# Performance work log

Measured on AMD Instinct MI355X. Metric: run time of the kernel, lower is better.

Reference implementation:

```python
import jax, jax.numpy as jnp
import numpy as np

IMG = 128
HW = IMG // 2          # render resolution (img_size // 2)
NPTS = 64              # samples per ray
MIN_D, MAX_D = 1.2, 2.8
VOL_PHYS = 1.0         # physical volume size; voxel = VOL_PHYS / D
B, C, D = 8, 16, 64
EPS_EA = 1e-10         # pytorch3d EmissionAbsorption eps
BN_EPS = 1e-5


def setup_inputs():
    key = jax.random.key(0)
    ks = jax.random.split(key, 6)
    R = jnp.tile(jnp.eye(3, dtype=jnp.float32)[None], (B, 1, 1))
    T = jnp.tile(jnp.array([0.0, 0.0, 2.0], jnp.float32)[None], (B, 1))
    K = jnp.tile(jnp.array([[180.0, 0.0, 64.0], [0.0, 180.0, 64.0], [0.0, 0.0, 1.0]],
                           jnp.float32)[None], (B, 1, 1))
    feature_3d = jax.random.normal(ks[0], (B, C, D, D, D), jnp.float32)
    density_3d = jax.random.uniform(ks[1], (B, 1, D, D, D), jnp.float32)
    wt = jax.random.normal(ks[2], (16, 16, 6, 6), jnp.float32) * 0.05
    bt = jnp.zeros((16,), jnp.float32)
    g1 = jnp.ones((16,), jnp.float32); be1 = jnp.zeros((16,), jnp.float32)
    w1 = jax.random.normal(ks[3], (8, 16, 5, 5), jnp.float32) * 0.05
    b1 = jnp.zeros((8,), jnp.float32)
    g2 = jnp.ones((8,), jnp.float32); be2 = jnp.zeros((8,), jnp.float32)
    w2 = jax.random.normal(ks[4], (3, 8, 5, 5), jnp.float32) * 0.05
    b2 = jnp.zeros((3,), jnp.float32)
    return dict(R=R, T=T, K=K, feature_3d=feature_3d, density_3d=density_3d,
                wt=wt, bt=bt, g1=g1, be1=be1, w1=w1, b1=b1, g2=g2, be2=be2,
                w2=w2, b2=b2)


def _trilerp(vol, pts):
    # vol [C,Dz,Dy,Dx]; pts [N,3] xyz in [-1,1]; grid_sample align_corners=True, zero padding
    Cc, Dz, Dy, Dx = vol.shape
    ix = (pts[:, 0] + 1.0) * 0.5 * (Dx - 1)
    iy = (pts[:, 1] + 1.0) * 0.5 * (Dy - 1)
    iz = (pts[:, 2] + 1.0) * 0.5 * (Dz - 1)
    x0f = jnp.floor(ix); y0f = jnp.floor(iy); z0f = jnp.floor(iz)
    fx, fy, fz = ix - x0f, iy - y0f, iz - z0f
    x0 = x0f.astype(jnp.int32); y0 = y0f.astype(jnp.int32); z0 = z0f.astype(jnp.int32)
    out = jnp.zeros((Cc, pts.shape[0]), vol.dtype)
    for dz in (0, 1):
        for dy in (0, 1):
            for dx in (0, 1):
                xc, yc, zc = x0 + dx, y0 + dy, z0 + dz
                w = ((fx if dx else 1.0 - fx) * (fy if dy else 1.0 - fy)
                     * (fz if dz else 1.0 - fz))
                valid = ((xc >= 0) & (xc < Dx) & (yc >= 0) & (yc < Dy)
                         & (zc >= 0) & (zc < Dz))
                v = vol[:, jnp.clip(zc, 0, Dz - 1), jnp.clip(yc, 0, Dy - 1),
                        jnp.clip(xc, 0, Dx - 1)]
                out = out + (w * valid) * v
    return out  # [C,N]


def _bn(x, g, b):
    m = x.mean((0, 2, 3), keepdims=True)
    v = x.var((0, 2, 3), keepdims=True)
    return g[None, :, None, None] * (x - m) * jax.lax.rsqrt(v + BN_EPS) + b[None, :, None, None]


def _leaky(x):
    return jnp.where(x >= 0, x, 0.01 * x)


def _conv(x, w, b, pad):
    y = jax.lax.conv_general_dilated(x, w, (1, 1), [(pad, pad), (pad, pad)],
                                     dimension_numbers=('NCHW', 'OIHW', 'NCHW'))
    return y + b[None, :, None, None]


def _conv_t(x, w, b):
    # torch ConvTranspose2d(k=6, stride=2, pad=2) == dilated conv with flipped, io-swapped kernel
    wf = jnp.flip(w, (-2, -1)).transpose(1, 0, 2, 3)
    y = jax.lax.conv_general_dilated(x, wf, (1, 1), [(3, 3), (3, 3)],
                                     lhs_dilation=(2, 2),
                                     dimension_numbers=('NCHW', 'OIHW', 'NCHW'))
    return y + b[None, :, None, None]


def _forward(R, T, K, feature_3d, density_3d, wt, bt, g1, be1, w1, b1, g2, be2, w2, b2):
    Bb, Cc, Dv, Hv, Wv = feature_3d.shape
    # K /= 2; K[:,-1,-1] = 1 (non-mutating)
    Kh = (K / 2.0).at[:, 2, 2].set(1.0)
    fx, fy = Kh[:, 0, 0], Kh[:, 1, 1]
    cx, cy = Kh[:, 0, 2], Kh[:, 1, 2]
    # pixel-center grid at half resolution (NDCGridRaysampler pixel centers)
    u = jnp.arange(HW, dtype=jnp.float32) + 0.5
    v = jnp.arange(HW, dtype=jnp.float32) + 0.5
    ddx = (u[None, None, :] - cx[:, None, None]) / fx[:, None, None]  # [B,1,W]
    ddy = (v[None, :, None] - cy[:, None, None]) / fy[:, None, None]  # [B,H,1]
    one = jnp.ones((1, 1, 1), jnp.float32)
    dirs_cam = jnp.stack(jnp.broadcast_arrays(ddx, ddy, one), axis=-1)  # [B,H,W,3]
    dirs_w = jnp.einsum('bji,bhwj->bhwi', R, dirs_cam)                  # R^T d
    origin = -jnp.einsum('bji,bj->bi', R, T)                            # cam center
    depths = jnp.linspace(MIN_D, MAX_D, NPTS, dtype=jnp.float32)
    pts = (origin[:, None, None, None, :]
           + dirs_w[:, :, :, None, :] * depths[None, None, None, :, None])  # [B,H,W,P,3]
    # world -> Volumes local coords (align_corners=True span: voxel*(dim-1))
    voxel = VOL_PHYS / Dv
    scale = jnp.array([2.0 / (voxel * (Wv - 1)), 2.0 / (voxel * (Hv - 1)),
                       2.0 / (voxel * (Dv - 1))], jnp.float32)
    loc = (pts * scale).reshape(Bb, -1, 3)
    vol = jnp.concatenate([feature_3d, density_3d], axis=1)  # [B,C+1,D,H,W]
    samp = jax.vmap(_trilerp)(vol, loc)                      # [B,C+1,N]
    samp = samp.reshape(Bb, Cc + 1, HW, HW, NPTS)
    feats = jnp.moveaxis(samp[:, :Cc], 1, -1)                # [B,H,W,P,C]
    sigma = samp[:, Cc]                                      # [B,H,W,P]
    # EmissionAbsorption raymarcher (shifted cumprod, shift=1)
    cp = jnp.cumprod((1.0 + EPS_EA) - sigma, axis=-1)
    absorb = jnp.concatenate([jnp.ones_like(cp[..., :1]), cp[..., :-1]], axis=-1)
    wgt = sigma * absorb
    img = jnp.einsum('bhwp,bhwpc->bhwc', wgt, feats)
    opac = 1.0 - jnp.prod(1.0 - sigma, axis=-1)
    imgs = jnp.moveaxis(img, -1, 1)        # [B,C,HW,HW]
    sil = opac[:, None]                    # [B,1,HW,HW]
    # conv refine head
    x = _conv_t(imgs, wt, bt)              # [B,16,128,128]
    x = _leaky(_bn(x, g1, be1))
    x = _conv(x, w1, b1, pad=2)
    x = _leaky(_bn(x, g2, be2))
    x = _conv(x, w2, b2, pad=2)
    imgs_out = jax.nn.relu(x)
    sil_up = jax.image.resize(sil, (Bb, 1, IMG, IMG), 'bilinear')
    return imgs_out, sil_up


def reference(R, T, K, feature_3d, density_3d, wt, bt, g1, be1, w1, b1, g2, be2, w2, b2):
    return _forward(R, T, K, feature_3d, density_3d, wt, bt, g1, be1, w1, b1,
                    g2, be2, w2, b2)
```

## Files before the change

kernel.cpp:

```cpp
#include <hip/hip_runtime.h>
#include <hip/hip_bf16.h>

typedef __hip_bfloat16 bf16;
typedef unsigned int uint;
typedef unsigned short ushort;

using frag  = __attribute__((ext_vector_type(8))) short;
using f32x4 = __attribute__((ext_vector_type(4))) float;

__device__ bf16  g_volT[8ULL*262144*16];
__device__ bf16  g_imgT[8*4096*16];
__device__ bf16  g_t1 [8*16384*16];
__device__ bf16  g_a2r[8*16384*8];
__device__ float g_sil[8*4096];
__device__ float g_part [512*32];
__device__ float g_part2[256*16];
__device__ float g_stats[96];
__device__ bf16  g_wAt[4*5*64*8];
__device__ bf16  g_wA1[13*64*8];
__device__ bf16  g_wA2[7*64*8];

__device__ __forceinline__ float bup(ushort u){ union{uint u; float f;} x; x.u = ((uint)u)<<16; return x.f; }
__device__ __forceinline__ ushort bdn(float f){ union{ bf16 h; ushort s;} v; v.h = __float2bfloat16(f); return v.s; }
__device__ __forceinline__ uint aff2(uint u, float a0, float b0, float a1, float b1){
  float x0 = bup((ushort)(u & 0xffff)), x1 = bup((ushort)(u >> 16));
  float y0 = fmaf(a0, x0, b0); y0 = y0 >= 0.f ? y0 : 0.01f*y0;
  float y1 = fmaf(a1, x1, b1); y1 = y1 >= 0.f ? y1 : 0.01f*y1;
  return (uint)bdn(y0) | ((uint)bdn(y1) << 16);
}
__device__ __forceinline__ f32x4 mf(frag a, frag b, f32x4 c){
  return __builtin_amdgcn_mfma_f32_16x16x32_bf16(a, b, c, 0, 0, 0);
}
__device__ __forceinline__ void acc2(uint u, float w, float& a, float& b){
  union { uint u; float f; } lo, hi;
  lo.u = u << 16; hi.u = u & 0xffff0000u;
  a = fmaf(w, lo.f, a); b = fmaf(w, hi.f, b);
}

__global__ __launch_bounds__(256) void k_wprep(const float* __restrict__ wt,
                                               const float* __restrict__ w1,
                                               const float* __restrict__ w2)
{
  int tid = threadIdx.x;
  for (int idx = tid; idx < 4*5*64*8; idx += 256){
    int cls = idx / 2560; int rem = idx % 2560;
    int step = rem / 512; int rem2 = rem % 512;
    int lane = rem2 >> 3, j = rem2 & 7;
    int o = lane & 15;
    int k = step*32 + (lane>>4)*8 + j;
    int tau = k >> 4, ic = k & 15;
    int dr = cls >> 1, dc = cls & 1;
    float val = 0.f;
    if (tau < 9){
      int s = tau/3, t = tau%3;
      val = wt[(ic*16 + o)*36 + (4-2*s+dr)*6 + (4-2*t+dc)];
    }
    g_wAt[idx] = __float2bfloat16(val);
  }
  for (int idx = tid; idx < 13*64*8; idx += 256){
    int step = idx / 512; int rem2 = idx % 512;
    int lane = rem2 >> 3, j = rem2 & 7;
    int o = lane & 15;
    int k = step*32 + (lane>>4)*8 + j;
    int tau = k >> 4, ic = k & 15;
    float val = (tau < 25 && o < 8) ? w1[o*400 + ic*25 + tau] : 0.f;
    g_wA1[idx] = __float2bfloat16(val);
  }
  for (int idx = tid; idx < 7*64*8; idx += 256){
    int step = idx / 512; int rem2 = idx % 512;
    int lane = rem2 >> 3, j = rem2 & 7;
    int o = lane & 15;
    int k = step*32 + (lane>>4)*8 + j;
    int tau = k >> 3, ic = k & 7;
    float val = (tau < 25 && o < 3) ? w2[o*200 + ic*25 + tau] : 0.f;
    g_wA2[idx] = __float2bfloat16(val);
  }
}

__global__ __launch_bounds__(256) void k_transpose(const float* __restrict__ feat)
{
  __shared__ float lt[4*64*17];
  int blk = blockIdx.x;
  int yq = blk & 15, z = (blk>>4)&63, b = blk>>10;
  int y0 = yq*4;
  int tid = threadIdx.x;
  int xq = tid & 15;
  #pragma unroll
  for (int it=0; it<4; ++it){
    int cy = it*16 + (tid>>4);
    int c = cy >> 2, y = cy & 3;
    const float4 vv = *(const float4*)(feat + (size_t)b*4194304 + (size_t)c*262144
                                       + z*4096 + (y0+y)*64 + xq*4);
    float* dst = &lt[(y*64 + xq*4)*17 + c];
    dst[0]=vv.x; dst[17]=vv.y; dst[34]=vv.z; dst[51]=vv.w;
  }
  __syncthreads();
  int y = tid >> 6, x = tid & 63;
  const float* row = &lt[(y*64+x)*17];
  uint pk[8];
  #pragma unroll
  for (int c2=0;c2<8;c2++)
    pk[c2] = (uint)bdn(row[2*c2]) | ((uint)bdn(row[2*c2+1])<<16);
  uint* dst = (uint*)(g_volT + ((size_t)b*262144 + z*4096 + (y0+y)*64 + x)*16);
  uint4 lo; lo.x=pk[0]; lo.y=pk[1]; lo.z=pk[2]; lo.w=pk[3];
  uint4 hi; hi.x=pk[4]; hi.y=pk[5]; hi.z=pk[6]; hi.w=pk[7];
  *(uint4*)dst = lo;
  *(uint4*)(dst+4) = hi;
}

__global__ __launch_bounds__(64) void k_render(
    const float* __restrict__ R, const float* __restrict__ T, const float* __restrict__ Kin,
    const float* __restrict__ dens)
{
  int blk  = blockIdx.x;
  int lane = threadIdx.x;
  int b  = blk & 7;
  int t  = blk >> 3;
  int py0 = (t >> 3) * 8, px0 = (t & 7) * 8;
  int h = py0 + (lane >> 3), w = px0 + (lane & 7);

  float fx = Kin[b*9+0]*0.5f, fy = Kin[b*9+4]*0.5f;
  float cx = Kin[b*9+2]*0.5f, cy = Kin[b*9+5]*0.5f;
  float u = (float)w + 0.5f, v = (float)h + 0.5f;
  float dcx = (u - cx)/fx, dcy = (v - cy)/fy;
  float Rm[9];
  #pragma unroll
  for (int i=0;i<9;i++) Rm[i] = R[b*9+i];
  float T0 = T[b*3+0], T1 = T[b*3+1], T2 = T[b*3+2];
  float dwx = Rm[0]*dcx + Rm[3]*dcy + Rm[6];
  float dwy = Rm[1]*dcx + Rm[4]*dcy + Rm[7];
  float dwz = Rm[2]*dcx + Rm[5]*dcy + Rm[8];
  float ox = -(Rm[0]*T0 + Rm[3]*T1 + Rm[6]*T2);
  float oy = -(Rm[1]*T0 + Rm[4]*T1 + Rm[7]*T2);
  float oz = -(Rm[2]*T0 + Rm[5]*T1 + Rm[8]*T2);

  const float SC = 2.0f*64.0f/63.0f;
  const float* dp = dens + (size_t)b*262144;
  const bf16* vb = g_volT + (size_t)b*262144*16;

  float vch[16];
  #pragma unroll
  for (int c=0;c<16;c++) vch[c] = 0.f;
  float Trun = 1.0f, Pop = 1.0f;

  for (int d=0; d<64; ++d){
    float depth = 1.2f + (1.6f/63.0f) * (float)d;
    float ix = (ox + dwx*depth)*SC;  ix = (ix + 1.0f)*0.5f*63.0f;
    float iy = (oy + dwy*depth)*SC;  iy = (iy + 1.0f)*0.5f*63.0f;
    float iz = (oz + dwz*depth)*SC;  iz = (iz + 1.0f)*0.5f*63.0f;
    float xf = floorf(ix), yf = floorf(iy), zf = floorf(iz);
    int x0 = (int)xf, y0 = (int)yf, z0 = (int)zf;
    float sigma = 0.f;

    bool anyv = (x0>=-1)&(x0<64)&(y0>=-1)&(y0<64)&(z0>=-1)&(z0<64);
    if (anyv){
      float fxr = ix-xf, fyr = iy-yf, fzr = iz-zf;
      int offs[8]; float cw[8];
      #pragma unroll
      for (int k=0;k<8;k++){
        int dx = k&1, dy=(k>>1)&1, dz=(k>>2)&1;
        int xc=x0+dx, yc=y0+dy, zc=z0+dz;
        bool valid = (xc>=0)&(xc<64)&(yc>=0)&(yc<64)&(zc>=0)&(zc<64);
        float wk = (dx?fxr:1.f-fxr)*(dy?fyr:1.f-fyr)*(dz?fzr:1.f-fzr);
        cw[k] = valid ? wk : 0.0f;
        int xcc = min(max(xc,0),63), ycc=min(max(yc,0),63), zcc=min(max(zc,0),63);
        offs[k] = (zcc*64 + ycc)*64 + xcc;
      }
      #pragma unroll
      for (int k=0;k<8;k++) sigma += cw[k]*dp[offs[k]];

      float wgt = sigma * Trun;
      if (wgt > 1e-7f){
        #pragma unroll
        for (int k=0;k<8;k++){
          const uint4* p = (const uint4*)(vb + (size_t)offs[k]*16);
          uint4 q0 = p[0];
          uint4 q1 = p[1];
          float wk = cw[k]*wgt;
          acc2(q0.x, wk, vch[0],  vch[1]);
          acc2(q0.y, wk, vch[2],  vch[3]);
          acc2(q0.z, wk, vch[4],  vch[5]);
          acc2(q0.w, wk, vch[6],  vch[7]);
          acc2(q1.x, wk, vch[8],  vch[9]);
          acc2(q1.y, wk, vch[10], vch[11]);
          acc2(q1.z, wk, vch[12], vch[13]);
          acc2(q1.w, wk, vch[14], vch[15]);
        }
      }
    }
    Trun *= (1.0f + 1e-10f - sigma);
    Pop  *= (1.0f - sigma);
    if (__ballot(Trun > 1e-7f) == 0ULL) break;
  }

  g_sil[b*4096 + h*64 + w] = 1.0f - Pop;
  uint pk[8];
  #pragma unroll
  for (int c2=0;c2<8;c2++)
    pk[c2] = (uint)bdn(vch[2*c2]) | ((uint)bdn(vch[2*c2+1])<<16);
  uint* dst = (uint*)(g_imgT + ((size_t)(b*4096) + h*64 + w)*16);
  uint4 lo; lo.x=pk[0]; lo.y=pk[1]; lo.z=pk[2]; lo.w=pk[3];
  uint4 hi; hi.x=pk[4]; hi.y=pk[5]; hi.z=pk[6]; hi.w=pk[7];
  *(uint4*)dst = lo;
  *(uint4*)(dst+4) = hi;
}

__global__ __launch_bounds__(256) void k_convt(const float* __restrict__ bt)
{
  __shared__ __align__(16) short tile[3*66*16];
  __shared__ float ssum[4][16], ssq[4][16];

  int blk = blockIdx.x;
  int r = blk & 63, b = blk >> 6;
  int tid = threadIdx.x;

  for (int idx = tid; idx < 396; idx += 256){
    int row3 = idx / 132; int rem = idx - row3*132;
    int c2 = rem >> 1, half = rem & 1;
    int gr = r - 1 + row3, gc = c2 - 1;
    uint4 val = make_uint4(0,0,0,0);
    if (gr>=0 && gr<64 && gc>=0 && gc<64)
      val = *(const uint4*)(g_imgT + ((size_t)(b*4096) + gr*64 + gc)*16 + half*8);
    *(uint4*)(tile + (row3*66 + c2)*16 + half*8) = val;
  }
  __syncthreads();

  int wv = tid >> 6, lane = tid & 63;
  int dr = wv >> 1, dc = wv & 1;
  int quad = lane >> 4, col = lane & 15;
  int ic0 = (quad & 1) * 8;

  f32x4 acc[4];
  #pragma unroll
  for (int n=0;n<4;n++) acc[n] = (f32x4){0.f,0.f,0.f,0.f};

  #pragma unroll
  for (int s5=0; s5<5; ++s5){
    frag a = *(const frag*)(g_wAt + ((wv*5 + s5)*64 + lane)*8);
    int tau = 2*s5 + (quad >> 1);
    if (tau > 8) tau = 0;
    int ss = tau/3, tt = tau%3;
    #pragma unroll
    for (int n=0;n<4;n++){
      int c2 = n*16 + col + tt;
      frag bf = *(const frag*)(tile + (ss*66 + c2)*16 + ic0);
      acc[n] = mf(a, bf, acc[n]);
    }
  }

  float4 bo = *(const float4*)(bt + quad*4);
  float bor[4] = {bo.x, bo.y, bo.z, bo.w};
  float sv[4] = {0,0,0,0}, qv[4] = {0,0,0,0};
  int orow = 2*r + dr;
  #pragma unroll
  for (int n=0;n<4;n++){
    int ocol = 2*(n*16 + col) + dc;
    bf16* dst = g_t1 + ((size_t)(b*128 + orow)*128 + ocol)*16 + quad*4;
    #pragma unroll
    for (int reg=0;reg<4;reg++){
      float vvv = acc[n][reg] + bor[reg];
      dst[reg] = __float2bfloat16(vvv);
      sv[reg] += vvv; qv[reg] += vvv*vvv;
    }
  }
  #pragma unroll
  for (int m=1; m<16; m<<=1){
    #pragma unroll
    for (int reg=0;reg<4;reg++){
      sv[reg] += __shfl_xor(sv[reg], m, 64);
      qv[reg] += __shfl_xor(qv[reg], m, 64);
    }
  }
  if ((lane & 15) == 0){
    #pragma unroll
    for (int reg=0;reg<4;reg++){
      ssum[wv][quad*4+reg] = sv[reg];
      ssq [wv][quad*4+reg] = qv[reg];
    }
  }
  __syncthreads();
  if (tid < 16){
    g_part[blk*32 + tid]      = ssum[0][tid]+ssum[1][tid]+ssum[2][tid]+ssum[3][tid];
    g_part[blk*32 + 16 + tid] = ssq[0][tid]+ssq[1][tid]+ssq[2][tid]+ssq[3][tid];
  }
}

__global__ __launch_bounds__(256) void k_fin1(const float* __restrict__ g,
                                              const float* __restrict__ be)
{
  __shared__ float rs[256], rq[256];
  int tid = threadIdx.x; int c = tid>>4, seg = tid&15;
  float s=0.f, q=0.f;
  for (int k=0;k<32;k++){
    int blk = seg*32+k;
    s += g_part[blk*32 + c];
    q += g_part[blk*32 + 16 + c];
  }
  rs[tid]=s; rq[tid]=q; __syncthreads();
  for (int sft=8; sft>0; sft>>=1){
    if (seg<sft){ rs[tid]+=rs[tid+sft]; rq[tid]+=rq[tid+sft]; }
    __syncthreads();
  }
  if (seg==0){
    float m = rs[tid]*(1.0f/131072.f);
    float v = rq[tid]*(1.0f/131072.f) - m*m;
    float a = g[c]*rsqrtf(v+1e-5f);
    g_stats[32+c] = a; g_stats[48+c] = be[c]-m*a;
  }
}

__global__ __launch_bounds__(256) void k_fin2(const float* __restrict__ g,
                                              const float* __restrict__ be)
{
  __shared__ float rs[256], rq[256];
  int tid = threadIdx.x; int seg = tid & 31, c = tid >> 5;
  float s=0.f, q=0.f;
  for (int k=0;k<8;k++){
    int blk = seg*8+k;
    s += g_part2[blk*16 + c];
    q += g_part2[blk*16 + 8 + c];
  }
  rs[tid]=s; rq[tid]=q; __syncthreads();
  for (int sft=16; sft>0; sft>>=1){
    if (seg<sft){ rs[tid]+=rs[tid+sft]; rq[tid]+=rq[tid+sft]; }
    __syncthreads();
  }
  if (seg==0){
    float m = rs[tid]*(1.0f/131072.f);
    float v = rq[tid]*(1.0f/131072.f) - m*m;
    float a = g[c]*rsqrtf(v+1e-5f);
    g_stats[80+c] = a; g_stats[88+c] = be[c]-m*a;
  }
}

__global__ __launch_bounds__(256) void k_conv1(const float* __restrict__ b1)
{
  __shared__ __align__(16) short tile[8*132*16];
  __shared__ float ssum[4][8], ssq[4][8];

  int blk = blockIdx.x;
  int rt = blk & 31, b = blk >> 5;
  int tid = threadIdx.x;

  float pa[16], pb[16];
  #pragma unroll
  for (int c=0;c<16;c++){ pa[c] = g_stats[32+c]; pb[c] = g_stats[48+c]; }

  for (int it=0; it<5; ++it){
    int idx = it*256 + tid;
    if (idx < 1056){
      int r8 = idx / 132; int c2 = idx - r8*132;
      int gr = rt*4 - 2 + r8, gc = c2 - 2;
      uint4 v0 = make_uint4(0,0,0,0), v1 = make_uint4(0,0,0,0);
      if (gr>=0 && gr<128 && gc>=0 && gc<128){
        const bf16* src = g_t1 + ((size_t)(b*128 + gr)*128 + gc)*16;
        v0 = *(const uint4*)(src);
        v1 = *(const uint4*)(src + 8);
        v0.x = aff2(v0.x, pa[0],pb[0],pa[1],pb[1]);
        v0.y = aff2(v0.y, pa[2],pb[2],pa[3],pb[3]);
        v0.z = aff2(v0.z, pa[4],pb[4],pa[5],pb[5]);
        v0.w = aff2(v0.w, pa[6],pb[6],pa[7],pb[7]);
        v1.x = aff2(v1.x, pa[8],pb[8],pa[9],pb[9]);
        v1.y = aff2(v1.y, pa[10],pb[10],pa[11],pb[11]);
        v1.z = aff2(v1.z, pa[12],pb[12],pa[13],pb[13]);
        v1.w = aff2(v1.w, pa[14],pb[14],pa[15],pb[15]);
      }
      *(uint4*)(tile + (r8*132 + c2)*16)     = v0;
      *(uint4*)(tile + (r8*132 + c2)*16 + 8) = v1;
    }
  }
  __syncthreads();

  int wv = tid >> 6, lane = tid & 63;
  int quad = lane >> 4, col = lane & 15;
  int ic0 = (quad & 1) * 8;

  f32x4 acc[8];
  #pragma unroll
  for (int n=0;n<8;n++) acc[n] = (f32x4){0.f,0.f,0.f,0.f};

  for (int s13=0; s13<13; ++s13){
    frag a = *(const frag*)(g_wA1 + (s13*64 + lane)*8);
    int tau = 2*s13 + (quad >> 1);
    if (tau > 24) tau = 0;
    int dh = tau/5, dw = tau%5;
    int rowt = wv + dh;
    #pragma unroll
    for (int n=0;n<8;n++){
      int c2 = n*16 + col + dw;
      frag bf = *(const frag*)(tile + (rowt*132 + c2)*16 + ic0);
      acc[n] = mf(a, bf, acc[n]);
    }
  }

  int row = rt*4 + wv;
  float sv[4] = {0,0,0,0}, qv[4] = {0,0,0,0};
  if (quad < 2){
    float4 bo = *(const float4*)(b1 + quad*4);
    float bor[4] = {bo.x, bo.y, bo.z, bo.w};
    #pragma unroll
    for (int n=0;n<8;n++){
      int px = n*16 + col;
      bf16* dst = g_a2r + ((size_t)(b*128 + row)*128 + px)*8 + quad*4;
      #pragma unroll
      for (int reg=0;reg<4;reg++){
        float vvv = acc[n][reg] + bor[reg];
        dst[reg] = __float2bfloat16(vvv);
        sv[reg] += vvv; qv[reg] += vvv*vvv;
      }
    }
  }
  #pragma unroll
  for (int m=1; m<16; m<<=1){
    #pragma unroll
    for (int reg=0;reg<4;reg++){
      sv[reg] += __shfl_xor(sv[reg], m, 64);
      qv[reg] += __shfl_xor(qv[reg], m, 64);
    }
  }
  if ((lane & 15) == 0 && quad < 2){
    #pragma unroll
    for (int reg=0;reg<4;reg++){
      ssum[wv][quad*4+reg] = sv[reg];
      ssq [wv][quad*4+reg] = qv[reg];
    }
  }
  __syncthreads();
  if (tid < 8){
    g_part2[blk*16 + tid]     = ssum[0][tid]+ssum[1][tid]+ssum[2][tid]+ssum[3][tid];
    g_part2[blk*16 + 8 + tid] = ssq[0][tid]+ssq[1][tid]+ssq[2][tid]+ssq[3][tid];
  }
}

__global__ __launch_bounds__(256) void k_conv2(float* __restrict__ outp,
                                               const float* __restrict__ b2)
{
  __shared__ __align__(16) short tile[8*132*8];

  int blk = blockIdx.x;
  int rt = blk & 31, b = blk >> 5;
  int tid = threadIdx.x;

  float pa[8], pb[8];
  #pragma unroll
  for (int c=0;c<8;c++){ pa[c] = g_stats[80+c]; pb[c] = g_stats[88+c]; }

  for (int it=0; it<5; ++it){
    int idx = it*256 + tid;
    if (idx < 1056){
      int r8 = idx / 132; int c2 = idx - r8*132;
      int gr = rt*4 - 2 + r8, gc = c2 - 2;
      uint4 v0 = make_uint4(0,0,0,0);
      if (gr>=0 && gr<128 && gc>=0 && gc<128){
        v0 = *(const uint4*)(g_a2r + ((size_t)(b*128 + gr)*128 + gc)*8);
        v0.x = aff2(v0.x, pa[0],pb[0],pa[1],pb[1]);
        v0.y = aff2(v0.y, pa[2],pb[2],pa[3],pb[3]);
        v0.z = aff2(v0.z, pa[4],pb[4],pa[5],pb[5]);
        v0.w = aff2(v0.w, pa[6],pb[6],pa[7],pb[7]);
      }
      *(uint4*)(tile + (r8*132 + c2)*8) = v0;
    }
  }
  __syncthreads();

  int wv = tid >> 6, lane = tid & 63;
  int quad = lane >> 4, col = lane & 15;

  f32x4 acc[8];
  #pragma unroll
  for (int n=0;n<8;n++) acc[n] = (f32x4){0.f,0.f,0.f,0.f};

  for (int s7=0; s7<7; ++s7){
    frag a = *(const frag*)(g_wA2 + (s7*64 + lane)*8);
    int tau = 4*s7 + quad;
    if (tau > 24) tau = 0;
    int dh = tau/5, dw = tau%5;
    int rowt = wv + dh;
    #pragma unroll
    for (int n=0;n<8;n++){
      int c2 = n*16 + col + dw;
      frag bf = *(const frag*)(tile + (rowt*132 + c2)*8);
      acc[n] = mf(a, bf, acc[n]);
    }
  }

  if (quad == 0){
    int row = rt*4 + wv;
    float b2v[3] = {b2[0], b2[1], b2[2]};
    #pragma unroll
    for (int n=0;n<8;n++){
      int px = n*16 + col;
      #pragma unroll
      for (int reg=0;reg<3;reg++){
        float vvv = fmaxf(acc[n][reg] + b2v[reg], 0.f);
        outp[(size_t)(b*3 + reg)*16384 + row*128 + px] = vvv;
      }
    }
  }
}

__global__ __launch_bounds__(256) void k_silup(float* __restrict__ outp)
{
  int idx = blockIdx.x*256 + threadIdx.x;
  if (idx >= 8*16384) return;
  int b = idx >> 14;
  int y = (idx >> 7) & 127;
  int x = idx & 127;
  float sy = y*0.5f - 0.25f, sx = x*0.5f - 0.25f;
  float yfl = floorf(sy), xfl = floorf(sx);
  float fy = sy - yfl, fx = sx - xfl;
  int y0 = min(max((int)yfl,0),63), y1 = min(max((int)yfl+1,0),63);
  int x0 = min(max((int)xfl,0),63), x1 = min(max((int)xfl+1,0),63);
  const float* s = g_sil + b*4096;
  float vv = (1.f-fy)*((1.f-fx)*s[y0*64+x0] + fx*s[y0*64+x1])
           +      fy *((1.f-fx)*s[y1*64+x0] + fx*s[y1*64+x1]);
  outp[idx] = vv;
}

extern "C" void kernel_launch(void* const* d_in, const int* in_sizes, int n_in,
                              void* d_out, int out_size, void* d_ws, size_t ws_size,
                              hipStream_t stream)
{
  const float* R    = (const float*)d_in[0];
  const float* T    = (const float*)d_in[1];
  const float* K    = (const float*)d_in[2];
  const float* feat = (const float*)d_in[3];
  const float* dens = (const float*)d_in[4];
  const float* wt   = (const float*)d_in[5];
  const float* bt   = (const float*)d_in[6];
  const float* g1   = (const float*)d_in[7];
  const float* be1  = (const float*)d_in[8];
  const float* w1   = (const float*)d_in[9];
  const float* b1   = (const float*)d_in[10];
  const float* g2   = (const float*)d_in[11];
  const float* be2  = (const float*)d_in[12];
  const float* w2   = (const float*)d_in[13];
  const float* b2   = (const float*)d_in[14];

  k_wprep    <<<1, 256, 0, stream>>>(wt, w1, w2);
  k_transpose<<<8192, 256, 0, stream>>>(feat);
  k_render   <<<512, 64, 0, stream>>>(R, T, K, dens);
  k_convt    <<<512, 256, 0, stream>>>(bt);
  k_fin1     <<<1, 256, 0, stream>>>(g1, be1);
  k_conv1    <<<256, 256, 0, stream>>>(b1);
  k_fin2     <<<1, 256, 0, stream>>>(g2, be2);
  k_conv2    <<<256, 256, 0, stream>>>((float*)d_out, b2);
  k_silup    <<<512, 256, 0, stream>>>((float*)d_out + 393216);
}
```

Baseline: 334.6 us.

## Cull volume transpose to frustum bounds and fold small kernels into neighbors

```diff
diff --git a/kernel.cpp b/kernel.cpp
--- a/kernel.cpp
+++ b/kernel.cpp
@@ -19,6 +19,7 @@
 __device__ bf16  g_wAt[4*5*64*8];
 __device__ bf16  g_wA1[13*64*8];
 __device__ bf16  g_wA2[7*64*8];
+__device__ uint  g_ctr1, g_ctr2;
 
 __device__ __forceinline__ float bup(ushort u){ union{uint u; float f;} x; x.u = ((uint)u)<<16; return x.f; }
 __device__ __forceinline__ ushort bdn(float f){ union{ bf16 h; ushort s;} v; v.h = __float2bfloat16(f); return v.s; }
@@ -37,75 +38,114 @@
   a = fmaf(w, lo.f, a); b = fmaf(w, hi.f, b);
 }
 
-__global__ __launch_bounds__(256) void k_wprep(const float* __restrict__ wt,
-                                               const float* __restrict__ w1,
-                                               const float* __restrict__ w2)
-{
-  int tid = threadIdx.x;
-  for (int idx = tid; idx < 4*5*64*8; idx += 256){
-    int cls = idx / 2560; int rem = idx % 2560;
-    int step = rem / 512; int rem2 = rem % 512;
-    int lane = rem2 >> 3, j = rem2 & 7;
-    int o = lane & 15;
-    int k = step*32 + (lane>>4)*8 + j;
-    int tau = k >> 4, ic = k & 15;
-    int dr = cls >> 1, dc = cls & 1;
-    float val = 0.f;
-    if (tau < 9){
-      int s = tau/3, t = tau%3;
-      val = wt[(ic*16 + o)*36 + (4-2*s+dr)*6 + (4-2*t+dc)];
-    }
-    g_wAt[idx] = __float2bfloat16(val);
-  }
-  for (int idx = tid; idx < 13*64*8; idx += 256){
-    int step = idx / 512; int rem2 = idx % 512;
-    int lane = rem2 >> 3, j = rem2 & 7;
-    int o = lane & 15;
-    int k = step*32 + (lane>>4)*8 + j;
-    int tau = k >> 4, ic = k & 15;
-    float val = (tau < 25 && o < 8) ? w1[o*400 + ic*25 + tau] : 0.f;
-    g_wA1[idx] = __float2bfloat16(val);
-  }
-  for (int idx = tid; idx < 7*64*8; idx += 256){
-    int step = idx / 512; int rem2 = idx % 512;
-    int lane = rem2 >> 3, j = rem2 & 7;
-    int o = lane & 15;
-    int k = step*32 + (lane>>4)*8 + j;
-    int tau = k >> 3, ic = k & 7;
-    float val = (tau < 25 && o < 3) ? w2[o*200 + ic*25 + tau] : 0.f;
-    g_wA2[idx] = __float2bfloat16(val);
-  }
-}
-
-__global__ __launch_bounds__(256) void k_transpose(const float* __restrict__ feat)
+__global__ __launch_bounds__(256) void k_transpose(const float* __restrict__ feat,
+    const float* __restrict__ R, const float* __restrict__ T, const float* __restrict__ Kin,
+    const float* __restrict__ wt, const float* __restrict__ w1, const float* __restrict__ w2)
 {
   __shared__ float lt[4*64*17];
   int blk = blockIdx.x;
   int yq = blk & 15, z = (blk>>4)&63, b = blk>>10;
   int y0 = yq*4;
   int tid = threadIdx.x;
+
+  if (blk == 0){
+    if (tid == 0){ g_ctr1 = 0; g_ctr2 = 0; }
+    for (int idx = tid; idx < 4*5*64*8; idx += 256){
+      int cls = idx / 2560; int rem = idx % 2560;
+      int step = rem / 512; int rem2 = rem % 512;
+      int lane = rem2 >> 3, j = rem2 & 7;
+      int o = lane & 15;
+      int k = step*32 + (lane>>4)*8 + j;
+      int tau = k >> 4, ic = k & 15;
+      int dr = cls >> 1, dc = cls & 1;
+      float val = 0.f;
+      if (tau < 9){
+        int s = tau/3, t = tau%3;
+        val = wt[(ic*16 + o)*36 + (4-2*s+dr)*6 + (4-2*t+dc)];
+      }
+      g_wAt[idx] = __float2bfloat16(val);
+    }
+    for (int idx = tid; idx < 13*64*8; idx += 256){
+      int step = idx / 512; int rem2 = idx % 512;
+      int lane = rem2 >> 3, j = rem2 & 7;
+      int o = lane & 15;
+      int k = step*32 + (lane>>4)*8 + j;
+      int tau = k >> 4, ic = k & 15;
+      float val = (tau < 25 && o < 8) ? w1[o*400 + ic*25 + tau] : 0.f;
+      g_wA1[idx] = __float2bfloat16(val);
+    }
+    for (int idx = tid; idx < 7*64*8; idx += 256){
+      int step = idx / 512; int rem2 = idx % 512;
+      int lane = rem2 >> 3, j = rem2 & 7;
+      int o = lane & 15;
+      int k = step*32 + (lane>>4)*8 + j;
+      int tau = k >> 3, ic = k & 7;
+      float val = (tau < 25 && o < 3) ? w2[o*200 + ic*25 + tau] : 0.f;
+      g_wA2[idx] = __float2bfloat16(val);
+    }
+  }
+
+  float fx = Kin[b*9+0]*0.5f, fy = Kin[b*9+4]*0.5f;
+  float cx = Kin[b*9+2]*0.5f, cy = Kin[b*9+5]*0.5f;
+  float Rm[9];
+  #pragma unroll
+  for (int i=0;i<9;i++) Rm[i] = R[b*9+i];
+  float T0 = T[b*3+0], T1 = T[b*3+1], T2 = T[b*3+2];
+  float ox = -(Rm[0]*T0 + Rm[3]*T1 + Rm[6]*T2);
+  float oy = -(Rm[1]*T0 + Rm[4]*T1 + Rm[7]*T2);
+  float oz = -(Rm[2]*T0 + Rm[5]*T1 + Rm[8]*T2);
+  const float SC = 2.0f*64.0f/63.0f;
+  float xmn=1e30f,xmx=-1e30f,ymn=1e30f,ymx=-1e30f,zmn=1e30f,zmx=-1e30f;
+  #pragma unroll
+  for (int vtx=0; vtx<8; ++vtx){
+    float uu = (vtx&1)? 63.5f : 0.5f;
+    float vv = (vtx&2)? 63.5f : 0.5f;
+    float dd = (vtx&4)? 2.8f : 1.2f;
+    float dcx = (uu-cx)/fx, dcy = (vv-cy)/fy;
+    float dwx = Rm[0]*dcx + Rm[3]*dcy + Rm[6];
+    float dwy = Rm[1]*dcx + Rm[4]*dcy + Rm[7];
+    float dwz = Rm[2]*dcx + Rm[5]*dcy + Rm[8];
+    float gx = ((ox + dwx*dd)*SC + 1.0f)*31.5f;
+    float gy = ((oy + dwy*dd)*SC + 1.0f)*31.5f;
+    float gz = ((oz + dwz*dd)*SC + 1.0f)*31.5f;
+    xmn=fminf(xmn,gx); xmx=fmaxf(xmx,gx);
+    ymn=fminf(ymn,gy); ymx=fmaxf(ymx,gy);
+    zmn=fminf(zmn,gz); zmx=fmaxf(zmx,gz);
+  }
+  int xlo = max(0,(int)floorf(xmn)), xhi = min(63,(int)floorf(xmx)+1);
+  int ylo = max(0,(int)floorf(ymn)), yhi = min(63,(int)floorf(ymx)+1);
+  int zlo = max(0,(int)floorf(zmn)), zhi = min(63,(int)floorf(zmx)+1);
+
+  if (y0 > yhi || y0+3 < ylo || z > zhi || z < zlo) return;
+
   int xq = tid & 15;
+  bool okx = (xq*4 <= xhi) && (xq*4+3 >= xlo);
   #pragma unroll
   for (int it=0; it<4; ++it){
     int cy = it*16 + (tid>>4);
     int c = cy >> 2, y = cy & 3;
-    const float4 vv = *(const float4*)(feat + (size_t)b*4194304 + (size_t)c*262144
-                                       + z*4096 + (y0+y)*64 + xq*4);
-    float* dst = &lt[(y*64 + xq*4)*17 + c];
-    dst[0]=vv.x; dst[17]=vv.y; dst[34]=vv.z; dst[51]=vv.w;
+    if (okx){
+      const float4 vv = *(const float4*)(feat + (size_t)b*4194304 + (size_t)c*262144
+                                         + z*4096 + (y0+y)*64 + xq*4);
+      float* dst = &lt[(y*64 + xq*4)*17 + c];
+      dst[0]=vv.x; dst[17]=vv.y; dst[34]=vv.z; dst[51]=vv.w;
+    }
   }
   __syncthreads();
   int y = tid >> 6, x = tid & 63;
-  const float* row = &lt[(y*64+x)*17];
-  uint pk[8];
-  #pragma unroll
-  for (int c2=0;c2<8;c2++)
-    pk[c2] = (uint)bdn(row[2*c2]) | ((uint)bdn(row[2*c2+1])<<16);
-  uint* dst = (uint*)(g_volT + ((size_t)b*262144 + z*4096 + (y0+y)*64 + x)*16);
-  uint4 lo; lo.x=pk[0]; lo.y=pk[1]; lo.z=pk[2]; lo.w=pk[3];
-  uint4 hi; hi.x=pk[4]; hi.y=pk[5]; hi.z=pk[6]; hi.w=pk[7];
-  *(uint4*)dst = lo;
-  *(uint4*)(dst+4) = hi;
+  int xg = x >> 2;
+  if ((xg*4 <= xhi) && (xg*4+3 >= xlo)){
+    const float* row = &lt[(y*64+x)*17];
+    uint pk[8];
+    #pragma unroll
+    for (int c2=0;c2<8;c2++)
+      pk[c2] = (uint)bdn(row[2*c2]) | ((uint)bdn(row[2*c2+1])<<16);
+    uint* dst = (uint*)(g_volT + ((size_t)b*262144 + z*4096 + (y0+y)*64 + x)*16);
+    uint4 lo; lo.x=pk[0]; lo.y=pk[1]; lo.z=pk[2]; lo.w=pk[3];
+    uint4 hi; hi.x=pk[4]; hi.y=pk[5]; hi.z=pk[6]; hi.w=pk[7];
+    *(uint4*)dst = lo;
+    *(uint4*)(dst+4) = hi;
+  }
 }
 
 __global__ __launch_bounds__(64) void k_render(
@@ -205,10 +245,14 @@
   *(uint4*)(dst+4) = hi;
 }
 
-__global__ __launch_bounds__(256) void k_convt(const float* __restrict__ bt)
+__global__ __launch_bounds__(256) void k_convt(const float* __restrict__ bt,
+                                               const float* __restrict__ g1,
+                                               const float* __restrict__ be1)
 {
   __shared__ __align__(16) short tile[3*66*16];
   __shared__ float ssum[4][16], ssq[4][16];
+  __shared__ float rs[256], rq[256];
+  __shared__ uint s_done;
 
   int blk = blockIdx.x;
   int r = blk & 63, b = blk >> 6;
@@ -283,60 +327,41 @@
     g_part[blk*32 + tid]      = ssum[0][tid]+ssum[1][tid]+ssum[2][tid]+ssum[3][tid];
     g_part[blk*32 + 16 + tid] = ssq[0][tid]+ssq[1][tid]+ssq[2][tid]+ssq[3][tid];
   }
-}
-
-__global__ __launch_bounds__(256) void k_fin1(const float* __restrict__ g,
-                                              const float* __restrict__ be)
-{
-  __shared__ float rs[256], rq[256];
-  int tid = threadIdx.x; int c = tid>>4, seg = tid&15;
-  float s=0.f, q=0.f;
-  for (int k=0;k<32;k++){
-    int blk = seg*32+k;
-    s += g_part[blk*32 + c];
-    q += g_part[blk*32 + 16 + c];
-  }
-  rs[tid]=s; rq[tid]=q; __syncthreads();
-  for (int sft=8; sft>0; sft>>=1){
-    if (seg<sft){ rs[tid]+=rs[tid+sft]; rq[tid]+=rq[tid+sft]; }
-    __syncthreads();
-  }
-  if (seg==0){
-    float m = rs[tid]*(1.0f/131072.f);
-    float v = rq[tid]*(1.0f/131072.f) - m*m;
-    float a = g[c]*rsqrtf(v+1e-5f);
-    g_stats[32+c] = a; g_stats[48+c] = be[c]-m*a;
-  }
-}
-
-__global__ __launch_bounds__(256) void k_fin2(const float* __restrict__ g,
-                                              const float* __restrict__ be)
-{
-  __shared__ float rs[256], rq[256];
-  int tid = threadIdx.x; int seg = tid & 31, c = tid >> 5;
-  float s=0.f, q=0.f;
-  for (int k=0;k<8;k++){
-    int blk = seg*8+k;
-    s += g_part2[blk*16 + c];
-    q += g_part2[blk*16 + 8 + c];
-  }
-  rs[tid]=s; rq[tid]=q; __syncthreads();
-  for (int sft=16; sft>0; sft>>=1){
-    if (seg<sft){ rs[tid]+=rs[tid+sft]; rq[tid]+=rq[tid+sft]; }
-    __syncthreads();
-  }
-  if (seg==0){
-    float m = rs[tid]*(1.0f/131072.f);
-    float v = rq[tid]*(1.0f/131072.f) - m*m;
-    float a = g[c]*rsqrtf(v+1e-5f);
-    g_stats[80+c] = a; g_stats[88+c] = be[c]-m*a;
-  }
-}
-
-__global__ __launch_bounds__(256) void k_conv1(const float* __restrict__ b1)
+  __syncthreads();
+  __threadfence();
+  if (tid == 0) s_done = atomicAdd(&g_ctr1, 1u);
+  __syncthreads();
+  if (s_done == 511){
+    __threadfence();
+    int c = tid>>4, seg = tid&15;
+    float s=0.f, q=0.f;
+    for (int k=0;k<32;k++){
+      int bb = seg*32+k;
+      s += g_part[bb*32 + c];
+      q += g_part[bb*32 + 16 + c];
+    }
+    rs[tid]=s; rq[tid]=q; __syncthreads();
+    for (int sft=8; sft>0; sft>>=1){
+      if (seg<sft){ rs[tid]+=rs[tid+sft]; rq[tid]+=rq[tid+sft]; }
+      __syncthreads();
+    }
+    if (seg==0){
+      float m = rs[tid]*(1.0f/131072.f);
+      float v2 = rq[tid]*(1.0f/131072.f) - m*m;
+      float a = g1[c]*rsqrtf(v2+1e-5f);
+      g_stats[32+c] = a; g_stats[48+c] = be1[c]-m*a;
+    }
+  }
+}
+
+__global__ __launch_bounds__(256) void k_conv1(const float* __restrict__ b1,
+                                               const float* __restrict__ g2,
+                                               const float* __restrict__ be2)
 {
   __shared__ __align__(16) short tile[8*132*16];
   __shared__ float ssum[4][8], ssq[4][8];
+  __shared__ float rs[256], rq[256];
+  __shared__ uint s_done;
 
   int blk = blockIdx.x;
   int rt = blk & 31, b = blk >> 5;
@@ -430,6 +455,31 @@
     g_part2[blk*16 + tid]     = ssum[0][tid]+ssum[1][tid]+ssum[2][tid]+ssum[3][tid];
     g_part2[blk*16 + 8 + tid] = ssq[0][tid]+ssq[1][tid]+ssq[2][tid]+ssq[3][tid];
   }
+  __syncthreads();
+  __threadfence();
+  if (tid == 0) s_done = atomicAdd(&g_ctr2, 1u);
+  __syncthreads();
+  if (s_done == 255){
+    __threadfence();
+    int seg = tid & 31, c = tid >> 5;
+    float s=0.f, q=0.f;
+    for (int k=0;k<8;k++){
+      int bb = seg*8+k;
+      s += g_part2[bb*16 + c];
+      q += g_part2[bb*16 + 8 + c];
+    }
+    rs[tid]=s; rq[tid]=q; __syncthreads();
+    for (int sft=16; sft>0; sft>>=1){
+      if (seg<sft){ rs[tid]+=rs[tid+sft]; rq[tid]+=rq[tid+sft]; }
+      __syncthreads();
+    }
+    if (seg==0){
+      float m = rs[tid]*(1.0f/131072.f);
+      float v2 = rq[tid]*(1.0f/131072.f) - m*m;
+      float a = g2[c]*rsqrtf(v2+1e-5f);
+      g_stats[80+c] = a; g_stats[88+c] = be2[c]-m*a;
+    }
+  }
 }
 
 __global__ __launch_bounds__(256) void k_conv2(float* __restrict__ outp,
@@ -438,8 +488,26 @@
   __shared__ __align__(16) short tile[8*132*8];
 
   int blk = blockIdx.x;
+  int tid = threadIdx.x;
+
+  if (blk >= 256){
+    int idx = (blk-256)*256 + tid;
+    int b = idx >> 14;
+    int y = (idx >> 7) & 127;
+    int x = idx & 127;
+    float sy = y*0.5f - 0.25f, sx = x*0.5f - 0.25f;
+    float yfl = floorf(sy), xfl = floorf(sx);
+    float fy = sy - yfl, fxx = sx - xfl;
+    int y0 = min(max((int)yfl,0),63), y1 = min(max((int)yfl+1,0),63);
+    int x0 = min(max((int)xfl,0),63), x1 = min(max((int)xfl+1,0),63);
+    const float* s = g_sil + b*4096;
+    float vv = (1.f-fy)*((1.f-fxx)*s[y0*64+x0] + fxx*s[y0*64+x1])
+             +      fy *((1.f-fxx)*s[y1*64+x0] + fxx*s[y1*64+x1]);
+    outp[393216 + idx] = vv;
+    return;
+  }
+
   int rt = blk & 31, b = blk >> 5;
-  int tid = threadIdx.x;
 
   float pa[8], pb[8];
   #pragma unroll
@@ -497,24 +565,6 @@
       }
     }
   }
-}
-
-__global__ __launch_bounds__(256) void k_silup(float* __restrict__ outp)
-{
-  int idx = blockIdx.x*256 + threadIdx.x;
-  if (idx >= 8*16384) return;
-  int b = idx >> 14;
-  int y = (idx >> 7) & 127;
-  int x = idx & 127;
-  float sy = y*0.5f - 0.25f, sx = x*0.5f - 0.25f;
-  float yfl = floorf(sy), xfl = floorf(sx);
-  float fy = sy - yfl, fx = sx - xfl;
-  int y0 = min(max((int)yfl,0),63), y1 = min(max((int)yfl+1,0),63);
-  int x0 = min(max((int)xfl,0),63), x1 = min(max((int)xfl+1,0),63);
-  const float* s = g_sil + b*4096;
-  float vv = (1.f-fy)*((1.f-fx)*s[y0*64+x0] + fx*s[y0*64+x1])
-           +      fy *((1.f-fx)*s[y1*64+x0] + fx*s[y1*64+x1]);
-  outp[idx] = vv;
 }
 
 extern "C" void kernel_launch(void* const* d_in, const int* in_sizes, int n_in,
@@ -537,13 +587,9 @@
   const float* w2   = (const float*)d_in[13];
   const float* b2   = (const float*)d_in[14];
 
-  k_wprep    <<<1, 256, 0, stream>>>(wt, w1, w2);
-  k_transpose<<<8192, 256, 0, stream>>>(feat);
+  k_transpose<<<8192, 256, 0, stream>>>(feat, R, T, K, wt, w1, w2);
   k_render   <<<512, 64, 0, stream>>>(R, T, K, dens);
-  k_convt    <<<512, 256, 0, stream>>>(bt);
-  k_fin1     <<<1, 256, 0, stream>>>(g1, be1);
-  k_conv1    <<<256, 256, 0, stream>>>(b1);
-  k_fin2     <<<1, 256, 0, stream>>>(g2, be2);
-  k_conv2    <<<256, 256, 0, stream>>>((float*)d_out, b2);
-  k_silup    <<<512, 256, 0, stream>>>((float*)d_out + 393216);
-}
+  k_convt    <<<512, 256, 0, stream>>>(bt, g1, be1);
+  k_conv1    <<<256, 256, 0, stream>>>(b1, g2, be2);
+  k_conv2    <<<768, 256, 0, stream>>>((float*)d_out, b2);
+}
```

Result: slower. 386.2 us (+15.4%).
